# Performance work log

Measured on AMD Instinct MI355X. Metric: run time of the kernel, lower is better.

## Reference

```python
import jax, jax.numpy as jnp
import numpy as np
from jax import lax

B, CIN, COUT, H, W = 8, 128, 128, 128, 128
HID = COUT // 2  # expansion 0.5
K = 3            # kernel size
PAD = 1


def silu(v):
    return v * jax.nn.sigmoid(v)


def base_conv1x1(x, w, s, b):
    # 1x1 conv (no bias) + folded-BN affine (scale s, bias b) + SiLU
    y = jnp.einsum('bchw,oc->bohw', x, w)
    return silu(y * s[None, :, None, None] + b[None, :, None, None])


def bilinear_gather(img, py, px):
    Hin, Win = img.shape[1], img.shape[2]
    y0 = jnp.floor(py)
    x0 = jnp.floor(px)
    wy = py - y0
    wx = px - x0

    def corner(yc, xc):
        valid = (yc >= 0) & (yc <= Hin - 1) & (xc >= 0) & (xc <= Win - 1)
        yi = jnp.clip(yc, 0, Hin - 1).astype(jnp.int32)
        xi = jnp.clip(xc, 0, Win - 1).astype(jnp.int32)
        v = img[:, yi, xi]  # [C, Kk, H, W]
        return v * valid[None].astype(img.dtype)

    v00 = corner(y0, x0)
    v01 = corner(y0, x0 + 1)
    v10 = corner(y0 + 1, x0)
    v11 = corner(y0 + 1, x0 + 1)
    wy = wy[None]
    wx = wx[None]
    return (v00 * (1 - wy) * (1 - wx) + v01 * (1 - wy) * wx
            + v10 * wy * (1 - wx) + v11 * wy * wx)


def deform_conv_depthwise(x, off_w, off_b, dw):
    # x: [B, C, H, W]; off_w: [2*K*K, C, 3, 3]; dw: [C, K, K] (depthwise, groups=C)
    b, c, h, w = x.shape
    off = lax.conv_general_dilated(
        x, off_w, window_strides=(1, 1), padding=((PAD, PAD), (PAD, PAD)),
        dimension_numbers=('NCHW', 'OIHW', 'NCHW'))
    off = off + off_b[None, :, None, None]
    off = off.reshape(b, K * K, 2, h, w)  # torchvision: (dy, dx) per tap
    dy, dx = off[:, :, 0], off[:, :, 1]   # [B, 9, H, W]

    ky = jnp.repeat(jnp.arange(K, dtype=x.dtype), K)  # [9]
    kx = jnp.tile(jnp.arange(K, dtype=x.dtype), K)
    yy = jnp.arange(h, dtype=x.dtype)[None, :, None]  # [1, H, 1]
    xx = jnp.arange(w, dtype=x.dtype)[None, None, :]
    py = yy + ky[:, None, None] - PAD  # [9, H, W]
    px = xx + kx[:, None, None] - PAD
    py = py[None] + dy  # [B, 9, H, W]
    px = px[None] + dx

    sampled = jax.vmap(bilinear_gather)(x, py, px)  # [B, C, 9, H, W]
    return jnp.einsum('bckhw,ck->bchw', sampled, dw.reshape(c, K * K))


def setup_inputs() -> dict:
    key = jax.random.key(0)
    ks = jax.random.split(key, 12)
    f = jnp.float32
    inp = {
        'x': jax.random.normal(ks[0], (B, CIN, H, W), f),
        'w1': jax.random.normal(ks[1], (HID, CIN), f) * 0.05,
        's1': jnp.ones((HID,), f), 'b1': jnp.zeros((HID,), f),
        'w2': jax.random.normal(ks[2], (HID, CIN), f) * 0.05,
        's2': jnp.ones((HID,), f), 'b2': jnp.zeros((HID,), f),
        'w3': jax.random.normal(ks[3], (COUT, 2 * HID), f) * 0.05,
        's3': jnp.ones((COUT,), f), 'b3': jnp.zeros((COUT,), f),
        'off_w': jax.random.normal(ks[4], (2 * K * K, HID, K, K), f) * 0.01,
        'off_b': jnp.zeros((2 * K * K,), f),
        'dw': jax.random.normal(ks[5], (HID, K, K), f) * 0.1,
    }
    return inp


def reference(x, w1, s1, b1, w2, s2, b2, w3, s3, b3, off_w, off_b, dw):
    x1 = base_conv1x1(x, w1, s1, b1)          # [B, HID, H, W]
    x2 = base_conv1x1(x, w2, s2, b2)          # [B, HID, H, W]
    x1 = deform_conv_depthwise(x1, off_w, off_b, dw)
    xc = jnp.concatenate([x1, x2], axis=1)    # [B, 2*HID, H, W]
    return base_conv1x1(xc, w3, s3, b3)       # [B, COUT, H, W]
```

## Files before the change

kernel.cpp:

```cpp
#include <hip/hip_runtime.h>

typedef unsigned short u16;
typedef unsigned int   u32;

#define BB    8
#define CINC  128
#define HIDC  64
#define COUTC 128
#define HH    128
#define WWD   128
#define HWN   16384
#define NPOS  (BB*HWN)

typedef __attribute__((ext_vector_type(8))) short bf16x8;
typedef __attribute__((ext_vector_type(4))) float f32x4;

__device__ __forceinline__ float b2f(u16 u){
    union { u32 i; float f; } v; v.i = ((u32)u) << 16; return v.f;
}
__device__ __forceinline__ u16 f2b(float f){
    union { float f; u32 i; } v; v.f = f;
    u32 i = v.i;
    i += 0x7fffu + ((i >> 16) & 1u);
    return (u16)(i >> 16);
}
__device__ __forceinline__ float blo(u32 u){
    union { u32 i; float f; } v; v.i = u << 16; return v.f;
}
__device__ __forceinline__ float bhi(u32 u){
    union { u32 i; float f; } v; v.i = u & 0xFFFF0000u; return v.f;
}
__device__ __forceinline__ float silu(float y){
    return y / (1.f + __expf(-y));
}

template<bool ISB>
__device__ __forceinline__ float ldp(const void* p, int i){
    if (ISB) return b2f(((const u16*)p)[i]);
    return ((const float*)p)[i];
}

template<bool ISB>
__device__ __forceinline__ void k0_body(
    const void* w1, const void* s1, const void* b1,
    const void* w2, const void* s2, const void* b2,
    const void* w3, const void* s3, const void* b3,
    const void* offw, const void* offb, const void* dw,
    u16* __restrict__ wbc, u16* __restrict__ wb3,
    float* __restrict__ bfc, float* __restrict__ bf3,
    u16* __restrict__ wA, float* __restrict__ ob32, float* __restrict__ dwfT)
{
    int t = blockIdx.x*256 + threadIdx.x;
    if (t < 8192){
        wbc[t] = f2b(ldp<ISB>(w1,t) * ldp<ISB>(s1,t>>7));
    } else if (t < 16384){
        int u = t - 8192;
        wbc[t] = f2b(ldp<ISB>(w2,u) * ldp<ISB>(s2,u>>7));
    }
    if (t < 16384){
        wb3[t] = f2b(ldp<ISB>(w3,t) * ldp<ISB>(s3,t>>7));
    }
    if (t < 18432){
        int set  = t / 9216, rem = t % 9216;
        int tap  = rem / 1024; int rem2 = rem % 1024;
        int chunk= rem2 >> 9;  int rem3 = rem2 & 511;
        int lane = rem3 >> 3;  int jp   = rem3 & 7;
        int jg   = set*16 + (lane & 15);
        int c    = chunk*32 + (lane>>4)*8 + jp;
        float v  = (jg < 18) ? ldp<ISB>(offw, (jg*HIDC + c)*9 + tap) : 0.f;
        wA[t] = f2b(v);
    }
    if (t < HIDC)  bfc[t]      = ldp<ISB>(b1,t);
    if (t >= HIDC && t < 2*HIDC) bfc[t] = ldp<ISB>(b2,t-HIDC);
    if (t < COUTC) bf3[t] = ldp<ISB>(b3,t);
    if (t < 32)    ob32[t] = (t < 18) ? ldp<ISB>(offb,t) : 0.f;
    if (t < HIDC*9){
        int c = t / 9, k = t % 9;
        dwfT[k*HIDC + c] = ldp<ISB>(dw,t);
    }
}

__global__ __launch_bounds__(256) void k0_prep(
    const void* w1, const void* s1, const void* b1,
    const void* w2, const void* s2, const void* b2,
    const void* w3, const void* s3, const void* b3,
    const void* offw, const void* offb, const void* dw,
    u16* wbc, u16* wb3, float* bfc, float* bf3,
    u16* wA, float* ob32, float* dwfT)
{
    bool isb = (((const u32*)s1)[0] == 0x3F803F80u);
    if (isb) k0_body<true >(w1,s1,b1,w2,s2,b2,w3,s3,b3,offw,offb,dw,wbc,wb3,bfc,bf3,wA,ob32,dwfT);
    else     k0_body<false>(w1,s1,b1,w2,s2,b2,w3,s3,b3,offw,offb,dw,wbc,wb3,bfc,bf3,wA,ob32,dwfT);
}

template<bool ISB>
__device__ __forceinline__ void k1_body(const void* __restrict__ xv,
    const u16* __restrict__ wbc, const float* __restrict__ bfc,
    u16* __restrict__ x1, u16* __restrict__ x2)
{
    const int lane = threadIdx.x & 63;
    const int n    = lane & 15;
    const int quad = lane >> 4;
    bf16x8 w[8][4];
    #pragma unroll
    for (int mt = 0; mt < 8; ++mt)
        #pragma unroll
        for (int t = 0; t < 4; ++t)
            w[mt][t] = *(const bf16x8*)(wbc + (mt*16 + n)*CINC + t*32 + quad*8);
    float4 bias[8];
    #pragma unroll
    for (int mt = 0; mt < 8; ++mt)
        bias[mt] = *(const float4*)(bfc + mt*16 + quad*4);

    const int wv = blockIdx.x*4 + (threadIdx.x >> 6);
    for (int ci = wv; ci < NPOS/16; ci += gridDim.x*4){
        const int posbase = ci*16;
        const int bidx = posbase >> 14;
        const int hwb  = posbase & (HWN-1);
        f32x4 acc[8];
        #pragma unroll
        for (int mt = 0; mt < 8; ++mt) acc[mt] = (f32x4){0.f,0.f,0.f,0.f};
        #pragma unroll
        for (int t = 0; t < 4; ++t){
            bf16x8 bfr;
            if (ISB){
                const u16* xb = (const u16*)xv + (size_t)bidx*CINC*HWN + hwb + n;
                #pragma unroll
                for (int j = 0; j < 8; ++j)
                    bfr[j] = (short)xb[(size_t)(t*32 + quad*8 + j)*HWN];
            } else {
                const float* xb = (const float*)xv + (size_t)bidx*CINC*HWN + hwb + n;
                #pragma unroll
                for (int j = 0; j < 8; ++j)
                    bfr[j] = (short)f2b(xb[(size_t)(t*32 + quad*8 + j)*HWN]);
            }
            #pragma unroll
            for (int mt = 0; mt < 8; ++mt)
                acc[mt] = __builtin_amdgcn_mfma_f32_16x16x32_bf16(w[mt][t], bfr, acc[mt], 0,0,0);
        }
        const size_t rowb = (size_t)(posbase + n)*HIDC;
        #pragma unroll
        for (int mt = 0; mt < 8; ++mt){
            #pragma unroll
            for (int r = 0; r < 4; ++r){
                const int o = mt*16 + quad*4 + r;
                const u16 bv = f2b(silu(acc[mt][r] + bias[mt][r]));
                if (o < 64) x1[rowb + o]      = bv;
                else        x2[rowb + o - 64] = bv;
            }
        }
    }
}

__global__ __launch_bounds__(256, 2) void k1_mfma(const void* x, const u32* s1probe,
    const u16* wbc, const float* bfc, u16* x1, u16* x2)
{
    bool isb = (s1probe[0] == 0x3F803F80u);
    if (isb) k1_body<true >(x, wbc, bfc, x1, x2);
    else     k1_body<false>(x, wbc, bfc, x1, x2);
}

__global__ __launch_bounds__(256) void k2_mfma(const u16* __restrict__ x1,
    const u16* __restrict__ wA, const float* __restrict__ ob32,
    float* __restrict__ offT)
{
    const int lane = threadIdx.x & 63;
    const int n    = lane & 15;
    const int quad = lane >> 4;
    const int tile = blockIdx.x*4 + (threadIdx.x >> 6);
    const int posbase = tile*16;
    const int b   = posbase >> 14;
    const int hw  = posbase & (HWN-1);
    const int y   = hw >> 7;
    const int x0  = hw & (WWD-1);
    const int xb  = x0 + n - 1;
    const u16* bbase = x1 + (size_t)b*HWN*HIDC;

    f32x4 acc0 = (f32x4){0.f,0.f,0.f,0.f};
    f32x4 acc1 = (f32x4){0.f,0.f,0.f,0.f};

    #pragma unroll
    for (int ky = 0; ky < 3; ++ky){
        int ys = y + ky - 1;
        if ((unsigned)ys >= HH) continue;
        const u16* rowp = bbase + (size_t)ys*WWD*HIDC;
        #pragma unroll
        for (int kx = 0; kx < 3; ++kx){
            int  xs  = xb + kx;
            int  xcl = min(max(xs, 0), WWD-1);
            bool vx  = ((unsigned)xs < WWD);
            const int tap = ky*3 + kx;
            #pragma unroll
            for (int ch = 0; ch < 2; ++ch){
                bf16x8 bfr = *(const bf16x8*)(rowp + xcl*HIDC + ch*32 + quad*8);
                if (!vx) bfr = (bf16x8){0,0,0,0,0,0,0,0};
                bf16x8 a0 = *(const bf16x8*)(wA + ((0*9 + tap)*2 + ch)*512 + lane*8);
                bf16x8 a1 = *(const bf16x8*)(wA + ((1*9 + tap)*2 + ch)*512 + lane*8);
                acc0 = __builtin_amdgcn_mfma_f32_16x16x32_bf16(a0, bfr, acc0, 0,0,0);
                acc1 = __builtin_amdgcn_mfma_f32_16x16x32_bf16(a1, bfr, acc1, 0,0,0);
            }
        }
    }
    #pragma unroll
    for (int r = 0; r < 4; ++r){
        int j0 = quad*4 + r;
        offT[(size_t)j0*NPOS + posbase + n] = acc0[r] + ob32[j0];
        int j1 = 16 + quad*4 + r;
        if (j1 < 18)
            offT[(size_t)j1*NPOS + posbase + n] = acc1[r] + ob32[j1];
    }
}

__global__ __launch_bounds__(256) void k3a_prep(const float* __restrict__ offT,
    int* __restrict__ offsP, float4* __restrict__ facs)
{
    int t  = blockIdx.x*256 + threadIdx.x;
    int hw = t & (HWN-1);
    int y  = hw >> 7, x = hw & (WWD-1);
    #pragma unroll
    for (int k = 0; k < 9; ++k){
        float dy = offT[(size_t)(2*k  )*NPOS + t];
        float dx = offT[(size_t)(2*k+1)*NPOS + t];
        float py = (float)(y + k/3 - 1) + dy;
        float px = (float)(x + k%3 - 1) + dx;
        float fy = floorf(py), fx = floorf(px);
        float wy = py - fy,    wx = px - fx;
        int y0 = (int)fy, x0 = (int)fx;
        float vy0 = ((unsigned)y0     < HH)  ? 1.f : 0.f;
        float vy1 = ((unsigned)(y0+1) < HH)  ? 1.f : 0.f;
        float vx0 = ((unsigned)x0     < WWD) ? 1.f : 0.f;
        float vx1 = ((unsigned)(x0+1) < WWD) ? 1.f : 0.f;
        int yc0 = min(max(y0,   0), HH-1),  yc1 = min(max(y0+1, 0), HH-1);
        int xc0 = min(max(x0,   0), WWD-1), xc1 = min(max(x0+1, 0), WWD-1);
        float wy1 = 1.f - wy, wx1 = 1.f - wx;
        float4 w4;
        w4.x = wy1*wx1*vy0*vx0;
        w4.y = wy1*wx *vy0*vx1;
        w4.z = wy *wx1*vy1*vx0;
        w4.w = wy *wx *vy1*vx1;
        int o0 = (yc0*WWD + xc0)*HIDC;
        int sx = (xc1 != xc0) ? 1 : 0;
        int sy = (yc1 != yc0) ? 1 : 0;
        offsP[(size_t)t*9 + k] = o0 | (sx << 20) | (sy << 21);
        facs [(size_t)t*9 + k] = w4;
    }
}

__global__ __launch_bounds__(256, 2) void k3b_gather(const u16* __restrict__ x1,
    const int* __restrict__ offsP, const float4* __restrict__ facs,
    const float* __restrict__ dwfT, u16* __restrict__ x1d)
{
    const int tid  = blockIdx.x*256 + threadIdx.x;
    const int lane = tid & 63;
    const int wave = tid >> 6;
    const int li   = lane & 15;
    const int posw = wave << 2;
    const int pos  = posw + (lane >> 4);
    const int b    = posw >> 14;
    const u32* xb32 = (const u32*)(x1 + (size_t)b*HWN*HIDC) + li*2;

    const int*    op = offsP + (size_t)pos*9;
    const float4* fp = facs  + (size_t)pos*9;

    float acc0 = 0.f, acc1 = 0.f, acc2 = 0.f, acc3 = 0.f;

    #pragma unroll
    for (int k = 0; k < 9; ++k){
        const int    p   = op[k];
        const float4 f   = fp[k];
        const float4 dwf = *(const float4*)(dwfT + k*HIDC + li*4);
        const int o0  = (p & 0xFFFFF) >> 1;
        const int dxs = (p & (1<<20)) ? (HIDC>>1)       : 0;
        const int dys = (p & (1<<21)) ? ((WWD*HIDC)>>1) : 0;
        const uint2 q00 = *(const uint2*)(xb32 + o0);
        const uint2 q01 = *(const uint2*)(xb32 + o0 + dxs);
        const uint2 q10 = *(const uint2*)(xb32 + o0 + dys);
        const uint2 q11 = *(const uint2*)(xb32 + o0 + dys + dxs);

        float s0 = blo(q00.x)*f.x + blo(q01.x)*f.y + blo(q10.x)*f.z + blo(q11.x)*f.w;
        float s1 = bhi(q00.x)*f.x + bhi(q01.x)*f.y + bhi(q10.x)*f.z + bhi(q11.x)*f.w;
        float s2 = blo(q00.y)*f.x + blo(q01.y)*f.y + blo(q10.y)*f.z + blo(q11.y)*f.w;
        float s3 = bhi(q00.y)*f.x + bhi(q01.y)*f.y + bhi(q10.y)*f.z + bhi(q11.y)*f.w;
        acc0 += s0*dwf.x;
        acc1 += s1*dwf.y;
        acc2 += s2*dwf.z;
        acc3 += s3*dwf.w;
    }

    const u32 r0 = ((u32)f2b(acc1) << 16) | (u32)f2b(acc0);
    const u32 r1 = ((u32)f2b(acc3) << 16) | (u32)f2b(acc2);
    uint2* outp = (uint2*)((u32*)x1d + (size_t)pos*(HIDC/2) + li*2);
    *outp = make_uint2(r0, r1);
}

template<bool ISB>
__device__ __forceinline__ void k4_body(const u16* __restrict__ x1d,
    const u16* __restrict__ x2,
    const u16* __restrict__ wb3, const float* __restrict__ bf3,
    void* __restrict__ out)
{
    const int lane = threadIdx.x & 63;
    const int n    = lane & 15;
    const int quad = lane >> 4;
    bf16x8 w[8][4];
    #pragma unroll
    for (int mt = 0; mt < 8; ++mt)
        #pragma unroll
        for (int t = 0; t < 4; ++t)
            w[mt][t] = *(const bf16x8*)(wb3 + (mt*16 + n)*CINC + t*32 + quad*8);
    float4 bias[8];
    #pragma unroll
    for (int mt = 0; mt < 8; ++mt)
        bias[mt] = *(const float4*)(bf3 + mt*16 + quad*4);

    const int wv = blockIdx.x*4 + (threadIdx.x >> 6);
    for (int ci = wv; ci < NPOS/16; ci += gridDim.x*4){
        const int posbase = ci*16;
        const int bidx = posbase >> 14;
        const int hwb  = posbase & (HWN-1);
        f32x4 acc[8];
        #pragma unroll
        for (int mt = 0; mt < 8; ++mt) acc[mt] = (f32x4){0.f,0.f,0.f,0.f};
        const size_t rowb = (size_t)(posbase + n)*HIDC;
        #pragma unroll
        for (int t = 0; t < 4; ++t){
            const u16* src = (t < 2) ? x1d : x2;
            bf16x8 bfr = *(const bf16x8*)(src + rowb + (t&1)*32 + quad*8);
            #pragma unroll
            for (int mt = 0; mt < 8; ++mt)
                acc[mt] = __builtin_amdgcn_mfma_f32_16x16x32_bf16(w[mt][t], bfr, acc[mt], 0,0,0);
        }
        u16*   ob16 = (u16*)  out + (size_t)bidx*COUTC*HWN + hwb + n;
        float* obf  = (float*)out + (size_t)bidx*COUTC*HWN + hwb + n;
        #pragma unroll
        for (int mt = 0; mt < 8; ++mt){
            #pragma unroll
            for (int r = 0; r < 4; ++r){
                const int o = mt*16 + quad*4 + r;
                const float v = silu(acc[mt][r] + bias[mt][r]);
                if (ISB) ob16[(size_t)o*HWN] = f2b(v);
                else     obf [(size_t)o*HWN] = v;
            }
        }
    }
}

__global__ __launch_bounds__(256, 2) void k4_mfma(const u16* x1d, const u16* x2,
    const u32* s1probe, const u16* wb3, const float* bf3, void* out)
{
    bool isb = (s1probe[0] == 0x3F803F80u);
    if (isb) k4_body<true >(x1d, x2, wb3, bf3, out);
    else     k4_body<false>(x1d, x2, wb3, bf3, out);
}

extern "C" void kernel_launch(void* const* d_in, const int* in_sizes, int n_in,
                              void* d_out, int out_size, void* d_ws, size_t ws_size,
                              hipStream_t stream)
{
    const void* x    = d_in[0];
    const void* w1   = d_in[1];
    const void* s1   = d_in[2];
    const void* b1   = d_in[3];
    const void* w2   = d_in[4];
    const void* s2   = d_in[5];
    const void* b2   = d_in[6];
    const void* w3   = d_in[7];
    const void* s3   = d_in[8];
    const void* b3   = d_in[9];
    const void* offw = d_in[10];
    const void* offb = d_in[11];
    const void* dw   = d_in[12];

    char* ws = (char*)d_ws;
    u16*   x1    = (u16*)  (ws + 0);
    u16*   x2    = (u16*)  (ws + 16777216);
    u16*   x1d   = (u16*)  (ws + 33554432);
    float* offT  = (float*)(ws + 50331648);
    u16*   wbc   = (u16*)  (ws + 59768832);
    u16*   wb3   = (u16*)  (ws + 59801600);
    u16*   wA    = (u16*)  (ws + 59834368);
    float* dwfT  = (float*)(ws + 59871232);
    float* bfc   = (float*)(ws + 59873536);
    float* bf3   = (float*)(ws + 59874048);
    float* ob32  = (float*)(ws + 59874560);
    const size_t OFFSP_BYTES = (size_t)NPOS*9*4;
    const size_t BASE = 59875072;
    const size_t NEED = BASE + OFFSP_BYTES + (size_t)NPOS*9*16;
    int*    offsP;
    float4* facs;
    if (ws_size >= NEED){
        offsP = (int*)   (ws + BASE);
        facs  = (float4*)(ws + BASE + OFFSP_BYTES);
    } else {
        offsP = (int*)   d_out;
        facs  = (float4*)((char*)d_out + OFFSP_BYTES);
    }

    k0_prep<<<72, 256, 0, stream>>>(w1,s1,b1, w2,s2,b2, w3,s3,b3, offw,offb,dw,
                                    wbc, wb3, bfc, bf3, wA, ob32, dwfT);
    k1_mfma  <<<512, 256, 0, stream>>>(x, (const u32*)s1, wbc, bfc, x1, x2);
    k2_mfma  <<<2048, 256, 0, stream>>>(x1, wA, ob32, offT);
    k3a_prep <<<NPOS/256, 256, 0, stream>>>(offT, offsP, facs);
    k3b_gather<<<NPOS/16, 256, 0, stream>>>(x1, offsP, facs, dwfT, x1d);
    k4_mfma  <<<512, 256, 0, stream>>>(x1d, x2, (const u32*)s1, wb3, bf3, d_out);
}
```

Baseline: 275.4 us.

## Fuse offset prep into gather kernel and stage k1 outputs through LDS

Removes the separate k3a_prep kernel. The gather kernel now computes the bilinear offsets and corner weights itself into shared memory, and keeps the depthwise weights in LDS. This avoids writing and re-reading the large offsP/facs arrays through global memory. Separately, k1 now packs its bf16 outputs into a swizzled LDS tile and writes x1/x2 with coalesced 16-byte stores instead of scattered 2-byte stores. The cost is added LDS use and a block barrier in the gather kernel, with 9 of 16 lanes doing the prep work.

```diff
diff --git a/kernel.cpp b/kernel.cpp
--- a/kernel.cpp
+++ b/kernel.cpp
@@ -2,6 +2,7 @@
 
 typedef unsigned short u16;
 typedef unsigned int   u32;
+typedef unsigned char  u8;
 
 #define BB    8
 #define CINC  128
@@ -96,11 +97,12 @@
 template<bool ISB>
 __device__ __forceinline__ void k1_body(const void* __restrict__ xv,
     const u16* __restrict__ wbc, const float* __restrict__ bfc,
-    u16* __restrict__ x1, u16* __restrict__ x2)
+    u16* __restrict__ x1, u16* __restrict__ x2, u8* __restrict__ ldsb)
 {
     const int lane = threadIdx.x & 63;
     const int n    = lane & 15;
     const int quad = lane >> 4;
+    u8* mylds = ldsb + (threadIdx.x>>6)*4096;
     bf16x8 w[8][4];
     #pragma unroll
     for (int mt = 0; mt < 8; ++mt)
@@ -138,16 +140,23 @@
             for (int mt = 0; mt < 8; ++mt)
                 acc[mt] = __builtin_amdgcn_mfma_f32_16x16x32_bf16(w[mt][t], bfr, acc[mt], 0,0,0);
         }
-        const size_t rowb = (size_t)(posbase + n)*HIDC;
         #pragma unroll
         for (int mt = 0; mt < 8; ++mt){
-            #pragma unroll
-            for (int r = 0; r < 4; ++r){
-                const int o = mt*16 + quad*4 + r;
-                const u16 bv = f2b(silu(acc[mt][r] + bias[mt][r]));
-                if (o < 64) x1[rowb + o]      = bv;
-                else        x2[rowb + o - 64] = bv;
-            }
+            u32 lo = (u32)f2b(silu(acc[mt][0]+bias[mt].x)) | ((u32)f2b(silu(acc[mt][1]+bias[mt].y))<<16);
+            u32 hi = (u32)f2b(silu(acc[mt][2]+bias[mt].z)) | ((u32)f2b(silu(acc[mt][3]+bias[mt].w))<<16);
+            int chb = mt*32 + quad*8;
+            int sw  = chb ^ ((n&3)<<5);
+            *(uint2*)(mylds + n*256 + sw) = make_uint2(lo,hi);
+        }
+        #pragma unroll
+        for (int i = 0; i < 2; ++i){
+            int pp = i*8 + (lane>>3);
+            int cb = (lane&7)*16;
+            int sw = cb ^ ((pp&3)<<5);
+            uint4 v1 = *(const uint4*)(mylds + pp*256 + sw);
+            uint4 v2 = *(const uint4*)(mylds + pp*256 + 128 + sw);
+            *(uint4*)((char*)x1 + (size_t)(posbase+pp)*128 + cb) = v1;
+            *(uint4*)((char*)x2 + (size_t)(posbase+pp)*128 + cb) = v2;
         }
     }
 }
@@ -155,9 +164,10 @@
 __global__ __launch_bounds__(256, 2) void k1_mfma(const void* x, const u32* s1probe,
     const u16* wbc, const float* bfc, u16* x1, u16* x2)
 {
+    __shared__ u8 ldsb[4*4096];
     bool isb = (s1probe[0] == 0x3F803F80u);
-    if (isb) k1_body<true >(x, wbc, bfc, x1, x2);
-    else     k1_body<false>(x, wbc, bfc, x1, x2);
+    if (isb) k1_body<true >(x, wbc, bfc, x1, x2, ldsb);
+    else     k1_body<false>(x, wbc, bfc, x1, x2, ldsb);
 }
 
 __global__ __launch_bounds__(256) void k2_mfma(const u16* __restrict__ x1,
@@ -211,27 +221,42 @@
     }
 }
 
-__global__ __launch_bounds__(256) void k3a_prep(const float* __restrict__ offT,
-    int* __restrict__ offsP, float4* __restrict__ facs)
-{
-    int t  = blockIdx.x*256 + threadIdx.x;
-    int hw = t & (HWN-1);
-    int y  = hw >> 7, x = hw & (WWD-1);
-    #pragma unroll
-    for (int k = 0; k < 9; ++k){
-        float dy = offT[(size_t)(2*k  )*NPOS + t];
-        float dx = offT[(size_t)(2*k+1)*NPOS + t];
+__global__ __launch_bounds__(256, 2) void k3b_gather(const u16* __restrict__ x1,
+    const float* __restrict__ offT, const float* __restrict__ dwfT,
+    u16* __restrict__ x1d)
+{
+    __shared__ float s_dwf[576];
+    __shared__ __align__(16) u8 s_meta[16*208];
+
+    const int tid  = threadIdx.x;
+    if (tid < 144)
+        *(float4*)(s_dwf + tid*4) = *(const float4*)(dwfT + tid*4);
+
+    const int lane = tid & 63;
+    const int gw   = blockIdx.x*4 + (tid >> 6);
+    const int posw = gw << 2;
+    const int p    = lane >> 4;
+    const int li   = lane & 15;
+    const int pos  = posw + p;
+    const int slot = (tid >> 4) * 208;
+
+    if (li < 9){
+        const int k = li;
+        int hw = pos & (HWN-1);
+        int y  = hw >> 7, x = hw & (WWD-1);
+        float dy = offT[(size_t)(2*k  )*NPOS + pos];
+        float dx = offT[(size_t)(2*k+1)*NPOS + pos];
         float py = (float)(y + k/3 - 1) + dy;
         float px = (float)(x + k%3 - 1) + dx;
         float fy = floorf(py), fx = floorf(px);
         float wy = py - fy,    wx = px - fx;
-        int y0 = (int)fy, x0 = (int)fx;
-        float vy0 = ((unsigned)y0     < HH)  ? 1.f : 0.f;
-        float vy1 = ((unsigned)(y0+1) < HH)  ? 1.f : 0.f;
-        float vx0 = ((unsigned)x0     < WWD) ? 1.f : 0.f;
-        float vx1 = ((unsigned)(x0+1) < WWD) ? 1.f : 0.f;
+        int y0 = (int)fy, x0i = (int)fx;
+        float vy0 = ((unsigned)y0      < HH)  ? 1.f : 0.f;
+        float vy1 = ((unsigned)(y0+1)  < HH)  ? 1.f : 0.f;
+        float vx0 = ((unsigned)x0i     < WWD) ? 1.f : 0.f;
+        float vx1 = ((unsigned)(x0i+1) < WWD) ? 1.f : 0.f;
         int yc0 = min(max(y0,   0), HH-1),  yc1 = min(max(y0+1, 0), HH-1);
-        int xc0 = min(max(x0,   0), WWD-1), xc1 = min(max(x0+1, 0), WWD-1);
+        int xc0 = min(max(x0i,  0), WWD-1), xc1 = min(max(x0i+1, 0), WWD-1);
         float wy1 = 1.f - wy, wx1 = 1.f - wx;
         float4 w4;
         w4.x = wy1*wx1*vy0*vx0;
@@ -241,37 +266,23 @@
         int o0 = (yc0*WWD + xc0)*HIDC;
         int sx = (xc1 != xc0) ? 1 : 0;
         int sy = (yc1 != yc0) ? 1 : 0;
-        offsP[(size_t)t*9 + k] = o0 | (sx << 20) | (sy << 21);
-        facs [(size_t)t*9 + k] = w4;
-    }
-}
-
-__global__ __launch_bounds__(256, 2) void k3b_gather(const u16* __restrict__ x1,
-    const int* __restrict__ offsP, const float4* __restrict__ facs,
-    const float* __restrict__ dwfT, u16* __restrict__ x1d)
-{
-    const int tid  = blockIdx.x*256 + threadIdx.x;
-    const int lane = tid & 63;
-    const int wave = tid >> 6;
-    const int li   = lane & 15;
-    const int posw = wave << 2;
-    const int pos  = posw + (lane >> 4);
-    const int b    = posw >> 14;
+        *(int*)   (s_meta + slot + 4*k)       = o0 | (sx<<20) | (sy<<21);
+        *(float4*)(s_meta + slot + 48 + 16*k) = w4;
+    }
+    __syncthreads();
+
+    const int b = posw >> 14;
     const u32* xb32 = (const u32*)(x1 + (size_t)b*HWN*HIDC) + li*2;
 
-    const int*    op = offsP + (size_t)pos*9;
-    const float4* fp = facs  + (size_t)pos*9;
-
     float acc0 = 0.f, acc1 = 0.f, acc2 = 0.f, acc3 = 0.f;
-
     #pragma unroll
     for (int k = 0; k < 9; ++k){
-        const int    p   = op[k];
-        const float4 f   = fp[k];
-        const float4 dwf = *(const float4*)(dwfT + k*HIDC + li*4);
-        const int o0  = (p & 0xFFFFF) >> 1;
-        const int dxs = (p & (1<<20)) ? (HIDC>>1)       : 0;
-        const int dys = (p & (1<<21)) ? ((WWD*HIDC)>>1) : 0;
+        const int    pk  = *(const int*)   (s_meta + slot + 4*k);
+        const float4 f   = *(const float4*)(s_meta + slot + 48 + 16*k);
+        const float4 dwf = *(const float4*)(s_dwf + k*HIDC + li*4);
+        const int o0  = (pk & 0xFFFFF) >> 1;
+        const int dxs = (pk & (1<<20)) ? (HIDC>>1)       : 0;
+        const int dys = (pk & (1<<21)) ? ((WWD*HIDC)>>1) : 0;
         const uint2 q00 = *(const uint2*)(xb32 + o0);
         const uint2 q01 = *(const uint2*)(xb32 + o0 + dxs);
         const uint2 q10 = *(const uint2*)(xb32 + o0 + dys);
@@ -383,24 +394,11 @@
     float* bfc   = (float*)(ws + 59873536);
     float* bf3   = (float*)(ws + 59874048);
     float* ob32  = (float*)(ws + 59874560);
-    const size_t OFFSP_BYTES = (size_t)NPOS*9*4;
-    const size_t BASE = 59875072;
-    const size_t NEED = BASE + OFFSP_BYTES + (size_t)NPOS*9*16;
-    int*    offsP;
-    float4* facs;
-    if (ws_size >= NEED){
-        offsP = (int*)   (ws + BASE);
-        facs  = (float4*)(ws + BASE + OFFSP_BYTES);
-    } else {
-        offsP = (int*)   d_out;
-        facs  = (float4*)((char*)d_out + OFFSP_BYTES);
-    }
 
     k0_prep<<<72, 256, 0, stream>>>(w1,s1,b1, w2,s2,b2, w3,s3,b3, offw,offb,dw,
                                     wbc, wb3, bfc, bf3, wA, ob32, dwfT);
     k1_mfma  <<<512, 256, 0, stream>>>(x, (const u32*)s1, wbc, bfc, x1, x2);
     k2_mfma  <<<2048, 256, 0, stream>>>(x1, wA, ob32, offT);
-    k3a_prep <<<NPOS/256, 256, 0, stream>>>(offT, offsP, facs);
-    k3b_gather<<<NPOS/16, 256, 0, stream>>>(x1, offsP, facs, dwfT, x1d);
+    k3b_gather<<<NPOS/16, 256, 0, stream>>>(x1, offT, dwfT, x1d);
     k4_mfma  <<<512, 256, 0, stream>>>(x1d, x2, (const u32*)s1, wb3, bf3, d_out);
 }
```

New measurement: 258.2 us. -6.3%, faster.
